# Performance work log

Measured on AMD Instinct MI355X. Metric: run time of the kernel, lower is better.

Reference implementation:

```python
import jax, jax.numpy as jnp
import numpy as np

N = 50000      # nodes
E = 800000     # edges
IN = 256       # in_dim
H = 3          # num_heads
C = 64         # hidden_dim (per head)
D = H * C      # per-layer width = 192
OUT = 64       # out_dim
EPS_BN = 1e-5


def _gat_layer(h, W, att_src, att_dst, bias, src, dst):
    """PyG GATConv (concat=True, no self loops, eval/no dropout).
    h: [N, F_in], W: [F_in, H*C], att_src/att_dst: [H, C], bias: [H*C]."""
    x = (h @ W).reshape(-1, H, C)                       # [N, H, C]
    a_s = jnp.einsum('nhc,hc->nh', x, att_src)          # [N, H]
    a_d = jnp.einsum('nhc,hc->nh', x, att_dst)          # [N, H]
    e = jax.nn.leaky_relu(a_s[src] + a_d[dst], 0.2)     # [E, H]
    # segment softmax over incoming edges of each destination node
    m = jax.ops.segment_max(e, dst, num_segments=N)     # [N, H]
    m = jnp.where(jnp.isfinite(m), m, 0.0)
    w = jnp.exp(e - m[dst])                             # [E, H]
    den = jax.ops.segment_sum(w, dst, num_segments=N)   # [N, H]
    alpha = w / (den[dst] + 1e-16)                      # [E, H]
    out = jax.ops.segment_sum(x[src] * alpha[:, :, None], dst, num_segments=N)
    return out.reshape(-1, D) + bias                    # [N, H*C]


def _batchnorm(h, gamma, beta):
    mu = h.mean(0)
    var = h.var(0)
    return (h - mu) * jax.lax.rsqrt(var + EPS_BN) * gamma + beta


def setup_inputs() -> dict:
    key = jax.random.key(0)
    ks = jax.random.split(key, 16)
    s_in = 1.0 / np.sqrt(IN)
    s_d = 1.0 / np.sqrt(D)
    inp = {
        'x': jax.random.normal(ks[0], (N, IN), jnp.float32),
        'W1': jax.random.normal(ks[1], (IN, D), jnp.float32) * s_in,
        'att_src1': jax.random.normal(ks[2], (H, C), jnp.float32) * s_d,
        'att_dst1': jax.random.normal(ks[3], (H, C), jnp.float32) * s_d,
        'b1': jnp.zeros((D,), jnp.float32),
        'g1': jnp.ones((D,), jnp.float32),
        'beta1': jnp.zeros((D,), jnp.float32),
        'W2': jax.random.normal(ks[4], (D, D), jnp.float32) * s_d,
        'att_src2': jax.random.normal(ks[5], (H, C), jnp.float32) * s_d,
        'att_dst2': jax.random.normal(ks[6], (H, C), jnp.float32) * s_d,
        'b2': jnp.zeros((D,), jnp.float32),
        'g2': jnp.ones((D,), jnp.float32),
        'beta2': jnp.zeros((D,), jnp.float32),
        'Wf': jax.random.normal(ks[7], (D, OUT), jnp.float32) * s_d,
        'bf': jnp.zeros((OUT,), jnp.float32),
        'edge_index': jax.random.randint(ks[8], (2, E), 0, N, jnp.int64),
    }
    return inp


def reference(x, W1, att_src1, att_dst1, b1, g1, beta1,
              W2, att_src2, att_dst2, b2, g2, beta2,
              Wf, bf, edge_index):
    src, dst = edge_index[0], edge_index[1]
    h1 = _gat_layer(x, W1, att_src1, att_dst1, b1, src, dst)
    h1 = _batchnorm(jax.nn.relu(h1), g1, beta1)
    h2 = _gat_layer(h1, W2, att_src2, att_dst2, b2, src, dst)
    h2 = _batchnorm(jax.nn.relu(h2), g2, beta2)
    h_sum = h1 + h2
    return h_sum @ Wf + bf
```

## Files before the change

kernel.cpp:

```cpp
#include <hip/hip_runtime.h>

#define NN 50000
#define NE 800000
#define DIN 256
#define NH 3
#define HC 64
#define DD 192
#define DF 64
#define NB 196

typedef __attribute__((ext_vector_type(8))) short s8bf;
typedef __attribute__((ext_vector_type(8))) unsigned short u16x8;
typedef __attribute__((ext_vector_type(4))) float f32x4;

__device__ __forceinline__ unsigned short f2bf(float f) {
    unsigned u = __float_as_uint(f);
    unsigned r = u + 0x7fffu + ((u >> 16) & 1u);
    return (unsigned short)(r >> 16);
}
__device__ __forceinline__ float bf2f(unsigned short h) {
    return __uint_as_float(((unsigned)h) << 16);
}
__device__ __forceinline__ void split2(float f, unsigned short& h, unsigned short& l) {
    h = f2bf(f);
    l = f2bf(f - bf2f(h));
}
__device__ __forceinline__ float rl_f(float v, int j) {
    return __int_as_float(__builtin_amdgcn_readlane(__float_as_int(v), j));
}

#define W1G (DIN / 8 * DD)
#define W2G (DD / 8 * DD)
#define WFG (DD / 8 * DF)
__global__ __launch_bounds__(256)
void wsplit_all(const float* __restrict__ W1, const float* __restrict__ W2,
                const float* __restrict__ Wf,
                unsigned short* __restrict__ W1hT, unsigned short* __restrict__ W1lT,
                unsigned short* __restrict__ W2hT, unsigned short* __restrict__ W2lT,
                unsigned short* __restrict__ WfhT, unsigned short* __restrict__ WflT) {
    int idx = blockIdx.x * 256 + threadIdx.x;
    const float* W; unsigned short *Wh, *Wl; int K, D, base;
    if (idx < W1G)                  { W = W1; Wh = W1hT; Wl = W1lT; K = DIN; D = DD; base = idx; }
    else if (idx < W1G + W2G)       { W = W2; Wh = W2hT; Wl = W2lT; K = DD;  D = DD; base = idx - W1G; }
    else if (idx < W1G + W2G + WFG) { W = Wf; Wh = WfhT; Wl = WflT; K = DD;  D = DF; base = idx - W1G - W2G; }
    else return;
    int kb = base / D, d = base - kb * D;
    u16x8 hv, lv;
#pragma unroll
    for (int q = 0; q < 8; ++q) {
        unsigned short h, l;
        split2(W[(size_t)(kb * 8 + q) * D + d], h, l);
        hv[q] = h; lv[q] = l;
    }
    *(u16x8*)(Wh + (size_t)d * K + kb * 8) = hv;
    *(u16x8*)(Wl + (size_t)d * K + kb * 8) = lv;
}

template<int K, int DOUT, int MODE, bool DOTS>
__global__ __launch_bounds__(256)
void mfma_gemm(const float* __restrict__ A1, const float* __restrict__ A2,
               const float* __restrict__ bb1, const float* __restrict__ S1a_,
               const float* __restrict__ S2a_, const float* __restrict__ g1_,
               const float* __restrict__ be1_,
               const float* __restrict__ bb2, const float* __restrict__ S1b_,
               const float* __restrict__ S2b_, const float* __restrict__ g2_,
               const float* __restrict__ be2_,
               const unsigned short* __restrict__ BhT, const unsigned short* __restrict__ BlT,
               const float* __restrict__ att_s, const float* __restrict__ att_d,
               float4* __restrict__ as4o, float4* __restrict__ ad4o,
               const float* __restrict__ obias, float* __restrict__ Yf,
               unsigned short* __restrict__ Yb, int n) {
    constexpr int NT = DOUT / 64;
    constexpr int KB8 = K / 8;
    constexpr int NCF = (MODE == 2) ? 4 : (MODE == 1 ? 2 : 1);
    __shared__ unsigned short AH[64 * KB8 * 8];
    __shared__ float sdots[DOTS ? 4 : 1][64][6];
    __shared__ float cf[NCF][DD];

    const int tid = threadIdx.x;
    const int wave = tid >> 6, lane = tid & 63;
    const int r = lane & 15, kg = lane >> 4;
    const int row0 = blockIdx.x * 64;
    const int col0 = wave * (DOUT / 4);

    if constexpr (MODE >= 1) {
        if (tid < DD) {
            const float invn = 1.0f / NN;
            float mu = S1a_[tid] * invn;
            float var = S2a_[tid] * invn - mu * mu;
            float sc = g1_[tid] * rsqrtf(var + 1e-5f);
            cf[0][tid] = sc;
            cf[1][tid] = be1_[tid] - mu * sc;
            if constexpr (MODE == 2) {
                mu = S1b_[tid] * invn;
                var = S2b_[tid] * invn - mu * mu;
                sc = g2_[tid] * rsqrtf(var + 1e-5f);
                cf[2][tid] = sc;
                cf[3][tid] = be2_[tid] - mu * sc;
            }
        }
        __syncthreads();
    }

    constexpr int SIT = 64 * KB8 / 256;
    auto aoff = [&](int i) {
        int idx = tid + i * 256;
        int row = idx / KB8, kb = idx - row * KB8;
        int grow = min(row0 + row, n - 1);
        return (size_t)grow * K + kb * 8;
    };
    float4 cv0, cv1, cu0, cu1;
    {
        size_t o0 = aoff(0);
        cv0 = *(const float4*)(A1 + o0);
        cv1 = *(const float4*)(A1 + o0 + 4);
        if constexpr (MODE == 2) {
            cu0 = *(const float4*)(A2 + o0);
            cu1 = *(const float4*)(A2 + o0 + 4);
        }
    }
#pragma unroll
    for (int i = 0; i < SIT; ++i) {
        float4 nv0, nv1, nu0, nu1;
        if (i + 1 < SIT) {
            size_t on = aoff(i + 1);
            nv0 = *(const float4*)(A1 + on);
            nv1 = *(const float4*)(A1 + on + 4);
            if constexpr (MODE == 2) {
                nu0 = *(const float4*)(A2 + on);
                nu1 = *(const float4*)(A2 + on + 4);
            }
        }
        int idx = tid + i * 256;
        int row = idx / KB8, kb = idx - row * KB8;
        int j = kb * 8;
        float v[8];
        *(float4*)&v[0] = cv0; *(float4*)&v[4] = cv1;
        if constexpr (MODE >= 1) {
#pragma unroll
            for (int q = 0; q < 8; ++q)
                v[q] = fmaxf(v[q] + bb1[j + q], 0.f) * cf[0][j + q] + cf[1][j + q];
        }
        if constexpr (MODE == 2) {
            float u[8];
            *(float4*)&u[0] = cu0; *(float4*)&u[4] = cu1;
#pragma unroll
            for (int q = 0; q < 8; ++q)
                v[q] += fmaxf(u[q] + bb2[j + q], 0.f) * cf[2][j + q] + cf[3][j + q];
        }
        u16x8 hv;
#pragma unroll
        for (int q = 0; q < 8; ++q)
            hv[q] = f2bf(v[q]);
        int sw = kb ^ (row & 7);
        *(u16x8*)&AH[(row * KB8 + sw) * 8] = hv;
        cv0 = nv0; cv1 = nv1;
        if constexpr (MODE == 2) { cu0 = nu0; cu1 = nu1; }
    }
    __syncthreads();

    int boff[NT];
#pragma unroll
    for (int t = 0; t < NT; ++t)
        boff[t] = (col0 + t * 16 + r) * K + kg * 8;

    f32x4 acc[4][NT] = {};

    auto loadB = [&](int k0, s8bf* bh, s8bf* bl) {
#pragma unroll
        for (int t = 0; t < NT; ++t) {
            bh[t] = *(const s8bf*)(BhT + boff[t] + k0);
            bl[t] = *(const s8bf*)(BlT + boff[t] + k0);
        }
    };
    auto loadA = [&](int k0, s8bf* ah) {
        const int kb = k0 / 8 + kg;
#pragma unroll
        for (int g = 0; g < 4; ++g) {
            int row = g * 16 + r;
            int sw = kb ^ (row & 7);
            ah[g] = *(const s8bf*)&AH[(row * KB8 + sw) * 8];
        }
    };

    s8bf bh[NT], bl[NT], ah4[4];
    loadB(0, bh, bl);
    loadA(0, ah4);
#pragma unroll
    for (int k0 = 0; k0 < K; k0 += 32) {
        s8bf nbh[NT], nbl[NT], nah[4];
        if (k0 + 32 < K) {
            loadB(k0 + 32, nbh, nbl);
            loadA(k0 + 32, nah);
        }
#pragma unroll
        for (int g = 0; g < 4; ++g)
#pragma unroll
            for (int t = 0; t < NT; ++t) {
                acc[g][t] = __builtin_amdgcn_mfma_f32_16x16x32_bf16(ah4[g], bh[t], acc[g][t], 0, 0, 0);
                acc[g][t] = __builtin_amdgcn_mfma_f32_16x16x32_bf16(ah4[g], bl[t], acc[g][t], 0, 0, 0);
            }
#pragma unroll
        for (int t = 0; t < NT; ++t) { bh[t] = nbh[t]; bl[t] = nbl[t]; }
#pragma unroll
        for (int g = 0; g < 4; ++g) ah4[g] = nah[g];
    }

#pragma unroll
    for (int t = 0; t < NT; ++t) {
        int col = col0 + t * 16 + r;
        float b = (MODE == 2) ? obias[col] : 0.f;
#pragma unroll
        for (int g = 0; g < 4; ++g) {
#pragma unroll
            for (int rr = 0; rr < 4; ++rr) {
                int row = row0 + g * 16 + kg * 4 + rr;
                if (row < n) {
                    if constexpr (MODE == 2)
                        Yf[(size_t)row * DOUT + col] = acc[g][t][rr] + b;
                    else
                        Yb[(size_t)row * DOUT + col] = f2bf(acc[g][t][rr]);
                }
            }
        }
    }

    if constexpr (DOTS) {
        float asv[NT], adv[NT];
        int headt[NT];
#pragma unroll
        for (int t = 0; t < NT; ++t) {
            int col = col0 + t * 16 + r;
            asv[t] = att_s[col];
            adv[t] = att_d[col];
            headt[t] = (col0 + t * 16) >> 6;
        }
#pragma unroll
        for (int g = 0; g < 4; ++g) {
#pragma unroll
            for (int rr = 0; rr < 4; ++rr) {
                float rs0 = 0.f, rs1 = 0.f, rs2 = 0.f;
                float rd0 = 0.f, rd1 = 0.f, rd2 = 0.f;
#pragma unroll
                for (int t = 0; t < NT; ++t) {
                    float v = acc[g][t][rr];
                    float s = v * asv[t], dd = v * adv[t];
                    if (headt[t] == 0)      { rs0 += s; rd0 += dd; }
                    else if (headt[t] == 1) { rs1 += s; rd1 += dd; }
                    else                    { rs2 += s; rd2 += dd; }
                }
#pragma unroll
                for (int m = 1; m < 16; m <<= 1) {
                    rs0 += __shfl_xor(rs0, m); rs1 += __shfl_xor(rs1, m); rs2 += __shfl_xor(rs2, m);
                    rd0 += __shfl_xor(rd0, m); rd1 += __shfl_xor(rd1, m); rd2 += __shfl_xor(rd2, m);
                }
                if (r == 0) {
                    int row = g * 16 + kg * 4 + rr;
                    sdots[wave][row][0] = rs0; sdots[wave][row][1] = rs1; sdots[wave][row][2] = rs2;
                    sdots[wave][row][3] = rd0; sdots[wave][row][4] = rd1; sdots[wave][row][5] = rd2;
                }
            }
        }
        __syncthreads();
        if (tid < 64) {
            int row = row0 + tid;
            if (row < n) {
                float s0 = 0.f, s1 = 0.f, s2 = 0.f, d0 = 0.f, d1 = 0.f, d2 = 0.f;
#pragma unroll
                for (int w = 0; w < 4; ++w) {
                    s0 += sdots[w][tid][0]; s1 += sdots[w][tid][1]; s2 += sdots[w][tid][2];
                    d0 += sdots[w][tid][3]; d1 += sdots[w][tid][4]; d2 += sdots[w][tid][5];
                }
                as4o[row] = make_float4(s0, s1, s2, 0.f);
                ad4o[row] = make_float4(d0, d1, d2, 0.f);
            }
        }
    }
}

__global__ void hist_kernel(const int* __restrict__ dst, int* __restrict__ deg, int ne) {
    int e = blockIdx.x * blockDim.x + threadIdx.x;
    if (e < ne) atomicAdd(&deg[dst[e]], 1);
}

__global__ __launch_bounds__(256)
void blocksum_kernel(const int* __restrict__ deg, int* __restrict__ bsum) {
    int i = blockIdx.x * 256 + threadIdx.x;
    int v = (i < NN) ? deg[i] : 0;
#pragma unroll
    for (int off = 32; off; off >>= 1) v += __shfl_down(v, off);
    __shared__ int ws[4];
    if ((threadIdx.x & 63) == 0) ws[threadIdx.x >> 6] = v;
    __syncthreads();
    if (threadIdx.x == 0) bsum[blockIdx.x] = ws[0] + ws[1] + ws[2] + ws[3];
}

__global__ __launch_bounds__(256)
void scan_bsums(const int* __restrict__ bsum, int* __restrict__ boff,
                int* __restrict__ rowptr) {
    __shared__ int s[256];
    int t = threadIdx.x;
    int v = (t < NB) ? bsum[t] : 0;
    s[t] = v;
    __syncthreads();
    for (int off = 1; off < 256; off <<= 1) {
        int u = (t >= off) ? s[t - off] : 0;
        __syncthreads();
        s[t] += u;
        __syncthreads();
    }
    if (t < NB) boff[t] = s[t] - v;
    if (t == 255) rowptr[NN] = s[255];
}

__global__ __launch_bounds__(256)
void expand_kernel(const int* __restrict__ deg, const int* __restrict__ boff,
                   int* __restrict__ rowptr, int* __restrict__ cursor) {
    __shared__ int s[256];
    int t = threadIdx.x;
    int i = blockIdx.x * 256 + t;
    int v = (i < NN) ? deg[i] : 0;
    s[t] = v;
    __syncthreads();
    for (int off = 1; off < 256; off <<= 1) {
        int u = (t >= off) ? s[t - off] : 0;
        __syncthreads();
        s[t] += u;
        __syncthreads();
    }
    if (i < NN) {
        int excl = s[t] - v + boff[blockIdx.x];
        rowptr[i] = excl;
        cursor[i] = excl;
    }
}

__global__ void scatter_kernel(const int* __restrict__ src, const int* __restrict__ dst,
                               int* __restrict__ cursor, int* __restrict__ csr_src, int ne) {
    int e = blockIdx.x * blockDim.x + threadIdx.x;
    if (e >= ne) return;
    int d = dst[e];
    int pos = atomicAdd(&cursor[d], 1);
    csr_src[pos] = src[e];
}

__global__ __launch_bounds__(256)
void gat_gather(const unsigned short* __restrict__ xf,
                const float4* __restrict__ as4, const float4* __restrict__ ad4,
                const int* __restrict__ rowptr, const int* __restrict__ csr_src,
                float* __restrict__ outp) {
    int d = blockIdx.x * 4 + (threadIdx.x >> 6);
    if (d >= NN) return;
    const int lane = threadIdx.x & 63;
    const int beg = rowptr[d], end = rowptr[d + 1];
    const float4 adv = ad4[d];

    float a0 = 0.f, a1 = 0.f, a2 = 0.f;
    float den0 = 0.f, den1 = 0.f, den2 = 0.f;

    for (int base = beg; base < end; base += 64) {
        const int nb = min(64, end - base);
        int sl = 0;
        float w0 = 0.f, w1 = 0.f, w2 = 0.f;
        if (lane < nb) {
            sl = csr_src[base + lane];
            float4 av = as4[sl];
            float e0 = av.x + adv.x;
            float e1 = av.y + adv.y;
            float e2 = av.z + adv.z;
            e0 = e0 > 0.f ? e0 : 0.2f * e0;
            e1 = e1 > 0.f ? e1 : 0.2f * e1;
            e2 = e2 > 0.f ? e2 : 0.2f * e2;
            w0 = __expf(e0); w1 = __expf(e1); w2 = __expf(e2);
        }
        float r0 = w0, r1 = w1, r2 = w2;
#pragma unroll
        for (int off = 1; off < 64; off <<= 1) {
            r0 += __shfl_xor(r0, off);
            r1 += __shfl_xor(r1, off);
            r2 += __shfl_xor(r2, off);
        }
        den0 += r0; den1 += r1; den2 += r2;

        int j = 0;
        for (; j + 8 <= nb; j += 8) {
            const unsigned short* xp[8];
            float uw0[8], uw1[8], uw2[8];
#pragma unroll
            for (int k = 0; k < 8; ++k) {
                int s = __builtin_amdgcn_readlane(sl, j + k);
                xp[k] = xf + (size_t)s * DD;
                uw0[k] = rl_f(w0, j + k);
                uw1[k] = rl_f(w1, j + k);
                uw2[k] = rl_f(w2, j + k);
            }
            unsigned short f0[8], f1[8], f2[8];
#pragma unroll
            for (int k = 0; k < 8; ++k) {
                f0[k] = xp[k][lane];
                f1[k] = xp[k][64 + lane];
                f2[k] = xp[k][128 + lane];
            }
#pragma unroll
            for (int k = 0; k < 8; ++k) {
                a0 = fmaf(bf2f(f0[k]), uw0[k], a0);
                a1 = fmaf(bf2f(f1[k]), uw1[k], a1);
                a2 = fmaf(bf2f(f2[k]), uw2[k], a2);
            }
        }
        for (; j < nb; ++j) {
            int s = __builtin_amdgcn_readlane(sl, j);
            float u0 = rl_f(w0, j), u1 = rl_f(w1, j), u2 = rl_f(w2, j);
            const unsigned short* xp = xf + (size_t)s * DD;
            a0 = fmaf(bf2f(xp[lane]),       u0, a0);
            a1 = fmaf(bf2f(xp[64 + lane]),  u1, a1);
            a2 = fmaf(bf2f(xp[128 + lane]), u2, a2);
        }
    }
    size_t o = (size_t)d * DD + lane;
    outp[o]       = a0 / (den0 + 1e-16f);
    outp[o + 64]  = a1 / (den1 + 1e-16f);
    outp[o + 128] = a2 / (den2 + 1e-16f);
}

__global__ __launch_bounds__(192)
void bn_stats(const float* __restrict__ hbuf, const float* __restrict__ bias,
              float* __restrict__ s1, float* __restrict__ s2, int n) {
    int j = threadIdx.x;
    float b = bias[j];
    int r0 = blockIdx.x * 64;
    int r1 = min(r0 + 64, n);
    float a = 0.f, q = 0.f;
    for (int r = r0; r < r1; ++r) {
        float v = hbuf[(size_t)r * DD + j] + b;
        v = fmaxf(v, 0.f);
        a += v; q += v * v;
    }
    atomicAdd(&s1[j], a);
    atomicAdd(&s2[j], q);
}

extern "C" void kernel_launch(void* const* d_in, const int* in_sizes, int n_in,
                              void* d_out, int out_size, void* d_ws, size_t ws_size,
                              hipStream_t stream) {
    const float* x   = (const float*)d_in[0];
    const float* W1  = (const float*)d_in[1];
    const float* as1 = (const float*)d_in[2];
    const float* ad1 = (const float*)d_in[3];
    const float* b1  = (const float*)d_in[4];
    const float* g1  = (const float*)d_in[5];
    const float* be1 = (const float*)d_in[6];
    const float* W2  = (const float*)d_in[7];
    const float* as2 = (const float*)d_in[8];
    const float* ad2 = (const float*)d_in[9];
    const float* b2  = (const float*)d_in[10];
    const float* g2  = (const float*)d_in[11];
    const float* be2 = (const float*)d_in[12];
    const float* Wf  = (const float*)d_in[13];
    const float* bf  = (const float*)d_in[14];
    const int*   ei  = (const int*)d_in[15];
    const int* src = ei;
    const int* dst = ei + NE;
    float* out = (float*)d_out;

    float* ws = (float*)d_ws;
    float* CB1 = ws;
    float* CB2 = CB1 + (size_t)NN * DD;
    float4* AS4 = (float4*)(CB2 + (size_t)NN * DD);
    float4* AD4 = AS4 + NN;
    int* DEG   = (int*)(AD4 + NN);
    float* S1a = (float*)(DEG + NN);
    float* S2a = S1a + DD;
    float* S1b = S2a + DD;
    float* S2b = S1b + DD;
    float* SC1 = S2b + DD;
    float* SH1 = SC1 + DD;
    float* SC2 = SH1 + DD;
    float* SH2 = SC2 + DD;
    int* ROWPTR = (int*)(SH2 + DD);
    int* CURSOR = ROWPTR + NN + 1;
    int* BSUM   = CURSOR + NN;
    int* BOFF   = BSUM + NB;
    int* CSRS   = BOFF + NB;
    unsigned short* R    = (unsigned short*)(CSRS + NE);
    unsigned short* Abf  = R;
    unsigned short* W1hT = Abf + (size_t)NN * DD;
    unsigned short* W1lT = W1hT + DIN * DD;
    unsigned short* W2hT = W1lT + DIN * DD;
    unsigned short* W2lT = W2hT + DD * DD;
    unsigned short* WfhT = W2lT + DD * DD;
    unsigned short* WflT = WfhT + DD * DF;

    const int edge_grid = (NE + 255) / 256;
    const int gemm_grid = (NN + 63) / 64;
    const int gat_grid  = (NN + 3) / 4;
    const int bns_grid  = (NN + 63) / 64;
    const int wsp_grid  = (W1G + W2G + WFG + 255) / 256;

    hipMemsetAsync(DEG, 0, (size_t)NN * 4 + 4 * DD * 4, stream);

    hist_kernel<<<edge_grid, 256, 0, stream>>>(dst, DEG, NE);
    blocksum_kernel<<<NB, 256, 0, stream>>>(DEG, BSUM);
    scan_bsums<<<1, 256, 0, stream>>>(BSUM, BOFF, ROWPTR);
    expand_kernel<<<NB, 256, 0, stream>>>(DEG, BOFF, ROWPTR, CURSOR);
    scatter_kernel<<<edge_grid, 256, 0, stream>>>(src, dst, CURSOR, CSRS, NE);

    wsplit_all<<<wsp_grid, 256, 0, stream>>>(W1, W2, Wf, W1hT, W1lT, W2hT, W2lT, WfhT, WflT);

    mfma_gemm<DIN, DD, 0, true><<<gemm_grid, 256, 0, stream>>>(
        x, nullptr,
        nullptr, nullptr, nullptr, nullptr, nullptr,
        nullptr, nullptr, nullptr, nullptr, nullptr,
        W1hT, W1lT, as1, ad1, AS4, AD4, nullptr, nullptr, Abf, NN);
    gat_gather<<<gat_grid, 256, 0, stream>>>(Abf, AS4, AD4, ROWPTR, CSRS, CB1);
    bn_stats<<<bns_grid, 192, 0, stream>>>(CB1, b1, S1a, S2a, NN);

    mfma_gemm<DD, DD, 1, true><<<gemm_grid, 256, 0, stream>>>(
        CB1, nullptr,
        b1, S1a, S2a, g1, be1,
        nullptr, nullptr, nullptr, nullptr, nullptr,
        W2hT, W2lT, as2, ad2, AS4, AD4, nullptr, nullptr, Abf, NN);
    gat_gather<<<gat_grid, 256, 0, stream>>>(Abf, AS4, AD4, ROWPTR, CSRS, CB2);
    bn_stats<<<bns_grid, 192, 0, stream>>>(CB2, b2, S1b, S2b, NN);

    mfma_gemm<DD, DF, 2, false><<<gemm_grid, 256, 0, stream>>>(
        CB1, CB2,
        b1, S1a, S2a, g1, be1,
        b2, S1b, S2b, g2, be2,
        WfhT, WflT, nullptr, nullptr, nullptr, nullptr, bf, out, nullptr, NN);
}
```

Measured before the change: 405.5 us.

## Degree-sort destination nodes for gather balance and halve GEMM row tile

Builds a permutation of destination nodes bucketed by in-degree (descending, capped at 63) during the CSR construction, and has the attention gather kernel process nodes in that order so waves in a block see similar edge counts. Separately, the MFMA GEMM tile shrinks from 64 to 32 rows per block, doubling the grid for more occupancy and parallelism. It adds atomics in the scan kernels and an extra indirection per gather wave. The smaller tile also means each B-fragment load from global feeds fewer MFMAs.

```diff
diff --git a/kernel.cpp b/kernel.cpp
--- a/kernel.cpp
+++ b/kernel.cpp
@@ -73,14 +73,14 @@
     constexpr int NT = DOUT / 64;
     constexpr int KB8 = K / 8;
     constexpr int NCF = (MODE == 2) ? 4 : (MODE == 1 ? 2 : 1);
-    __shared__ unsigned short AH[64 * KB8 * 8];
-    __shared__ float sdots[DOTS ? 4 : 1][64][6];
+    __shared__ unsigned short AH[32 * KB8 * 8];
+    __shared__ float sdots[DOTS ? 4 : 1][32][6];
     __shared__ float cf[NCF][DD];
 
     const int tid = threadIdx.x;
     const int wave = tid >> 6, lane = tid & 63;
     const int r = lane & 15, kg = lane >> 4;
-    const int row0 = blockIdx.x * 64;
+    const int row0 = blockIdx.x * 32;
     const int col0 = wave * (DOUT / 4);
 
     if constexpr (MODE >= 1) {
@@ -102,7 +102,7 @@
         __syncthreads();
     }
 
-    constexpr int SIT = 64 * KB8 / 256;
+    constexpr int SIT = 32 * KB8 / 256;
     auto aoff = [&](int i) {
         int idx = tid + i * 256;
         int row = idx / KB8, kb = idx - row * KB8;
@@ -164,7 +164,7 @@
     for (int t = 0; t < NT; ++t)
         boff[t] = (col0 + t * 16 + r) * K + kg * 8;
 
-    f32x4 acc[4][NT] = {};
+    f32x4 acc[2][NT] = {};
 
     auto loadB = [&](int k0, s8bf* bh, s8bf* bl) {
 #pragma unroll
@@ -176,34 +176,34 @@
     auto loadA = [&](int k0, s8bf* ah) {
         const int kb = k0 / 8 + kg;
 #pragma unroll
-        for (int g = 0; g < 4; ++g) {
+        for (int g = 0; g < 2; ++g) {
             int row = g * 16 + r;
             int sw = kb ^ (row & 7);
             ah[g] = *(const s8bf*)&AH[(row * KB8 + sw) * 8];
         }
     };
 
-    s8bf bh[NT], bl[NT], ah4[4];
+    s8bf bh[NT], bl[NT], ah2[2];
     loadB(0, bh, bl);
-    loadA(0, ah4);
+    loadA(0, ah2);
 #pragma unroll
     for (int k0 = 0; k0 < K; k0 += 32) {
-        s8bf nbh[NT], nbl[NT], nah[4];
+        s8bf nbh[NT], nbl[NT], nah[2];
         if (k0 + 32 < K) {
             loadB(k0 + 32, nbh, nbl);
             loadA(k0 + 32, nah);
         }
 #pragma unroll
-        for (int g = 0; g < 4; ++g)
+        for (int g = 0; g < 2; ++g)
 #pragma unroll
             for (int t = 0; t < NT; ++t) {
-                acc[g][t] = __builtin_amdgcn_mfma_f32_16x16x32_bf16(ah4[g], bh[t], acc[g][t], 0, 0, 0);
-                acc[g][t] = __builtin_amdgcn_mfma_f32_16x16x32_bf16(ah4[g], bl[t], acc[g][t], 0, 0, 0);
+                acc[g][t] = __builtin_amdgcn_mfma_f32_16x16x32_bf16(ah2[g], bh[t], acc[g][t], 0, 0, 0);
+                acc[g][t] = __builtin_amdgcn_mfma_f32_16x16x32_bf16(ah2[g], bl[t], acc[g][t], 0, 0, 0);
             }
 #pragma unroll
         for (int t = 0; t < NT; ++t) { bh[t] = nbh[t]; bl[t] = nbl[t]; }
 #pragma unroll
-        for (int g = 0; g < 4; ++g) ah4[g] = nah[g];
+        for (int g = 0; g < 2; ++g) ah2[g] = nah[g];
     }
 
 #pragma unroll
@@ -211,7 +211,7 @@
         int col = col0 + t * 16 + r;
         float b = (MODE == 2) ? obias[col] : 0.f;
 #pragma unroll
-        for (int g = 0; g < 4; ++g) {
+        for (int g = 0; g < 2; ++g) {
 #pragma unroll
             for (int rr = 0; rr < 4; ++rr) {
                 int row = row0 + g * 16 + kg * 4 + rr;
@@ -236,7 +236,7 @@
             headt[t] = (col0 + t * 16) >> 6;
         }
 #pragma unroll
-        for (int g = 0; g < 4; ++g) {
+        for (int g = 0; g < 2; ++g) {
 #pragma unroll
             for (int rr = 0; rr < 4; ++rr) {
                 float rs0 = 0.f, rs1 = 0.f, rs2 = 0.f;
@@ -262,7 +262,7 @@
             }
         }
         __syncthreads();
-        if (tid < 64) {
+        if (tid < 32) {
             int row = row0 + tid;
             if (row < n) {
                 float s0 = 0.f, s1 = 0.f, s2 = 0.f, d0 = 0.f, d1 = 0.f, d2 = 0.f;
@@ -284,20 +284,28 @@
 }
 
 __global__ __launch_bounds__(256)
-void blocksum_kernel(const int* __restrict__ deg, int* __restrict__ bsum) {
-    int i = blockIdx.x * 256 + threadIdx.x;
+void blocksum_kernel(const int* __restrict__ deg, int* __restrict__ bsum,
+                     int* __restrict__ dhist) {
+    __shared__ int lh[64];
+    int tid = threadIdx.x;
+    if (tid < 64) lh[tid] = 0;
+    __syncthreads();
+    int i = blockIdx.x * 256 + tid;
     int v = (i < NN) ? deg[i] : 0;
-#pragma unroll
-    for (int off = 32; off; off >>= 1) v += __shfl_down(v, off);
+    if (i < NN) atomicAdd(&lh[63 - min(v, 63)], 1);
+    int s = v;
+#pragma unroll
+    for (int off = 32; off; off >>= 1) s += __shfl_down(s, off);
     __shared__ int ws[4];
-    if ((threadIdx.x & 63) == 0) ws[threadIdx.x >> 6] = v;
-    __syncthreads();
-    if (threadIdx.x == 0) bsum[blockIdx.x] = ws[0] + ws[1] + ws[2] + ws[3];
+    if ((tid & 63) == 0) ws[tid >> 6] = s;
+    __syncthreads();
+    if (tid == 0) bsum[blockIdx.x] = ws[0] + ws[1] + ws[2] + ws[3];
+    if (tid < 64 && lh[tid]) atomicAdd(&dhist[tid], lh[tid]);
 }
 
 __global__ __launch_bounds__(256)
 void scan_bsums(const int* __restrict__ bsum, int* __restrict__ boff,
-                int* __restrict__ rowptr) {
+                int* __restrict__ rowptr, int* __restrict__ dhist) {
     __shared__ int s[256];
     int t = threadIdx.x;
     int v = (t < NB) ? bsum[t] : 0;
@@ -311,15 +319,29 @@
     }
     if (t < NB) boff[t] = s[t] - v;
     if (t == 255) rowptr[NN] = s[255];
+    __syncthreads();
+    if (t < 64) {
+        int dv = dhist[t];
+        int ds = dv;
+#pragma unroll
+        for (int off = 1; off < 64; off <<= 1) {
+            int u = __shfl_up(ds, off);
+            if (t >= off) ds += u;
+        }
+        dhist[t] = ds - dv;
+    }
 }
 
 __global__ __launch_bounds__(256)
 void expand_kernel(const int* __restrict__ deg, const int* __restrict__ boff,
-                   int* __restrict__ rowptr, int* __restrict__ cursor) {
+                   int* __restrict__ rowptr, int* __restrict__ cursor,
+                   int* __restrict__ dhist, int* __restrict__ perm) {
     __shared__ int s[256];
+    __shared__ int lcnt[64], lbase[64];
     int t = threadIdx.x;
     int i = blockIdx.x * 256 + t;
     int v = (i < NN) ? deg[i] : 0;
+    if (t < 64) lcnt[t] = 0;
     s[t] = v;
     __syncthreads();
     for (int off = 1; off < 256; off <<= 1) {
@@ -328,10 +350,17 @@
         s[t] += u;
         __syncthreads();
     }
+    int b = 63 - min(v, 63);
+    int myidx = 0;
+    if (i < NN) myidx = atomicAdd(&lcnt[b], 1);
+    __syncthreads();
+    if (t < 64 && lcnt[t]) lbase[t] = atomicAdd(&dhist[t], lcnt[t]);
+    __syncthreads();
     if (i < NN) {
         int excl = s[t] - v + boff[blockIdx.x];
         rowptr[i] = excl;
         cursor[i] = excl;
+        perm[lbase[b] + myidx] = i;
     }
 }
 
@@ -348,9 +377,8 @@
 void gat_gather(const unsigned short* __restrict__ xf,
                 const float4* __restrict__ as4, const float4* __restrict__ ad4,
                 const int* __restrict__ rowptr, const int* __restrict__ csr_src,
-                float* __restrict__ outp) {
-    int d = blockIdx.x * 4 + (threadIdx.x >> 6);
-    if (d >= NN) return;
+                const int* __restrict__ perm, float* __restrict__ outp) {
+    const int d = perm[blockIdx.x * 4 + (threadIdx.x >> 6)];
     const int lane = threadIdx.x & 63;
     const int beg = rowptr[d], end = rowptr[d + 1];
     const float4 adv = ad4[d];
@@ -473,13 +501,11 @@
     float* S2a = S1a + DD;
     float* S1b = S2a + DD;
     float* S2b = S1b + DD;
-    float* SC1 = S2b + DD;
-    float* SH1 = SC1 + DD;
-    float* SC2 = SH1 + DD;
-    float* SH2 = SC2 + DD;
-    int* ROWPTR = (int*)(SH2 + DD);
+    int* DHIST  = (int*)(S2b + DD);
+    int* ROWPTR = DHIST + 64;
     int* CURSOR = ROWPTR + NN + 1;
-    int* BSUM   = CURSOR + NN;
+    int* PERM   = CURSOR + NN;
+    int* BSUM   = PERM + NN;
     int* BOFF   = BSUM + NB;
     int* CSRS   = BOFF + NB;
     unsigned short* R    = (unsigned short*)(CSRS + NE);
@@ -492,17 +518,17 @@
     unsigned short* WflT = WfhT + DD * DF;
 
     const int edge_grid = (NE + 255) / 256;
-    const int gemm_grid = (NN + 63) / 64;
-    const int gat_grid  = (NN + 3) / 4;
+    const int gemm_grid = (NN + 31) / 32;
+    const int gat_grid  = NN / 4;
     const int bns_grid  = (NN + 63) / 64;
     const int wsp_grid  = (W1G + W2G + WFG + 255) / 256;
 
-    hipMemsetAsync(DEG, 0, (size_t)NN * 4 + 4 * DD * 4, stream);
+    hipMemsetAsync(DEG, 0, (size_t)NN * 4 + 4 * DD * 4 + 64 * 4, stream);
 
     hist_kernel<<<edge_grid, 256, 0, stream>>>(dst, DEG, NE);
-    blocksum_kernel<<<NB, 256, 0, stream>>>(DEG, BSUM);
-    scan_bsums<<<1, 256, 0, stream>>>(BSUM, BOFF, ROWPTR);
-    expand_kernel<<<NB, 256, 0, stream>>>(DEG, BOFF, ROWPTR, CURSOR);
+    blocksum_kernel<<<NB, 256, 0, stream>>>(DEG, BSUM, DHIST);
+    scan_bsums<<<1, 256, 0, stream>>>(BSUM, BOFF, ROWPTR, DHIST);
+    expand_kernel<<<NB, 256, 0, stream>>>(DEG, BOFF, ROWPTR, CURSOR, DHIST, PERM);
     scatter_kernel<<<edge_grid, 256, 0, stream>>>(src, dst, CURSOR, CSRS, NE);
 
     wsplit_all<<<wsp_grid, 256, 0, stream>>>(W1, W2, Wf, W1hT, W1lT, W2hT, W2lT, WfhT, WflT);
@@ -512,7 +538,7 @@
         nullptr, nullptr, nullptr, nullptr, nullptr,
         nullptr, nullptr, nullptr, nullptr, nullptr,
         W1hT, W1lT, as1, ad1, AS4, AD4, nullptr, nullptr, Abf, NN);
-    gat_gather<<<gat_grid, 256, 0, stream>>>(Abf, AS4, AD4, ROWPTR, CSRS, CB1);
+    gat_gather<<<gat_grid, 256, 0, stream>>>(Abf, AS4, AD4, ROWPTR, CSRS, PERM, CB1);
     bn_stats<<<bns_grid, 192, 0, stream>>>(CB1, b1, S1a, S2a, NN);
 
     mfma_gemm<DD, DD, 1, true><<<gemm_grid, 256, 0, stream>>>(
@@ -520,7 +546,7 @@
         b1, S1a, S2a, g1, be1,
         nullptr, nullptr, nullptr, nullptr, nullptr,
         W2hT, W2lT, as2, ad2, AS4, AD4, nullptr, nullptr, Abf, NN);
-    gat_gather<<<gat_grid, 256, 0, stream>>>(Abf, AS4, AD4, ROWPTR, CSRS, CB2);
+    gat_gather<<<gat_grid, 256, 0, stream>>>(Abf, AS4, AD4, ROWPTR, CSRS, PERM, CB2);
     bn_stats<<<bns_grid, 192, 0, stream>>>(CB2, b2, S1b, S2b, NN);
 
     mfma_gemm<DD, DF, 2, false><<<gemm_grid, 256, 0, stream>>>(
```

After: 422.4 us. +4.2%, slower.
